# Kernel optimization log

Measured on AMD Instinct MI355X. Metric: run time of the kernel, lower is better.

Reference implementation:

```python
import jax, jax.numpy as jnp
import numpy as np

B, VOCAB, HIST, PEN_RANGE = 256, 128000, 512, 64


def setup_inputs() -> dict:
    key = jax.random.key(0)
    k1, k2, k3 = jax.random.split(key, 3)
    logits = jax.random.normal(k1, (B, VOCAB), dtype=jnp.float32)
    save_id = jax.random.randint(k2, (B, HIST), 0, VOCAB, dtype=jnp.int64)
    penalty_value = jax.random.uniform(k3, (1,), dtype=jnp.float32)
    return {
        "logits": logits,
        "save_id": save_id,
        "penalty_value": penalty_value,
        "penalty_range": PEN_RANGE,
    }


def reference(logits, save_id, penalty_value, penalty_range):
    # target_indices = save_id[:, -penalty_range:]  -> [B, R]
    idx = save_id[:, -penalty_range:]
    # gather logits at idx, multiply by penalty, scatter back (out-of-place)
    penalized = jnp.take_along_axis(logits, idx, axis=1) * penalty_value  # [B, R]
    rows = jnp.arange(logits.shape[0])[:, None]  # [B, 1]
    return logits.at[rows, idx].set(penalized)
```

## Files before the change

### kernel.cpp

```cpp
#include <hip/hip_runtime.h>

#define VOCAB 128000
#define HIST 512
#define ROW_F4 (VOCAB / 4)
#define CHUNKS_PER_ROW 8
#define CHUNK_F4 (ROW_F4 / CHUNKS_PER_ROW)
#define CHUNK_FLOATS (CHUNK_F4 * 4)

typedef float f32x4 __attribute__((ext_vector_type(4)));

__global__ __launch_bounds__(256)
void APPLY_PENALTY_5909874999394_fused(const f32x4* __restrict__ logits4,
                                       const float* __restrict__ logits,
                                       const int* __restrict__ save_id,
                                       const float* __restrict__ pval,
                                       const int* __restrict__ prange,
                                       f32x4* __restrict__ out4,
                                       float* __restrict__ out) {
    const int bid   = blockIdx.x;
    const int row   = bid >> 3;
    const int chunk = bid & 7;
    const long rowoff4 = (long)row * ROW_F4;
    const int  c0_4 = chunk * CHUNK_F4;

    for (int j = threadIdx.x; j < CHUNK_F4; j += 256) {
        f32x4 v = __builtin_nontemporal_load(&logits4[rowoff4 + c0_4 + j]);
        out4[rowoff4 + c0_4 + j] = v;
    }

    __syncthreads();

    const int pr = *prange;
    const float p = *pval;
    const int lo = c0_4 * 4;
    const int hi = lo + CHUNK_FLOATS;
    const int base = row * HIST + (HIST - pr);
    const long rowoff = (long)row * VOCAB;
    for (int k = threadIdx.x; k < pr; k += 256) {
        const int idx = save_id[base + k];
        if (idx >= lo && idx < hi)
            out[rowoff + idx] = logits[rowoff + idx] * p;
    }
}

extern "C" void kernel_launch(void* const* d_in, const int* in_sizes, int n_in,
                              void* d_out, int out_size, void* d_ws, size_t ws_size,
                              hipStream_t stream) {
    const float* logits  = (const float*)d_in[0];
    const int*   save_id = (const int*)d_in[1];
    const float* pval    = (const float*)d_in[2];
    const int*   prange  = (const int*)d_in[3];
    float* out = (float*)d_out;

    const int rows = out_size / VOCAB;
    const int grid = rows * CHUNKS_PER_ROW;
    APPLY_PENALTY_5909874999394_fused<<<grid, 256, 0, stream>>>(
        (const f32x4*)logits, logits, save_id, pval, prange,
        (f32x4*)out, out);
}
```

Baseline: 49.19 us.

## Apply penalty in-register via shared bitmap during single-pass copy

Each block first loads its share of the penalty indices and builds a shared-memory bitmap of which positions in its 5120-float chunk are penalized. It then streams the chunk once, multiplying the flagged lanes before storing. This removes the second scattered read-modify-write pass and the post-copy barrier, so each element is written only once. The grid also grows from 8 to 25 chunks per row with a fixed 5 float4 loads per thread. The index loading assumes penalty_range is at most 512, and the nontemporal load hint is dropped.

```diff
diff --git a/kernel.cpp b/kernel.cpp
--- a/kernel.cpp
+++ b/kernel.cpp
@@ -3,43 +3,62 @@
 #define VOCAB 128000
 #define HIST 512
 #define ROW_F4 (VOCAB / 4)
-#define CHUNKS_PER_ROW 8
-#define CHUNK_F4 (ROW_F4 / CHUNKS_PER_ROW)
+#define CHUNKS_PER_ROW 25
+#define CHUNK_F4 1280
 #define CHUNK_FLOATS (CHUNK_F4 * 4)
+#define CHUNK_WORDS (CHUNK_FLOATS / 32)
+#define F4_PER_THREAD 5
 
 typedef float f32x4 __attribute__((ext_vector_type(4)));
 
 __global__ __launch_bounds__(256)
 void APPLY_PENALTY_5909874999394_fused(const f32x4* __restrict__ logits4,
-                                       const float* __restrict__ logits,
                                        const int* __restrict__ save_id,
                                        const float* __restrict__ pval,
                                        const int* __restrict__ prange,
-                                       f32x4* __restrict__ out4,
-                                       float* __restrict__ out) {
+                                       f32x4* __restrict__ out4) {
     const int bid   = blockIdx.x;
-    const int row   = bid >> 3;
-    const int chunk = bid & 7;
-    const long rowoff4 = (long)row * ROW_F4;
-    const int  c0_4 = chunk * CHUNK_F4;
-
-    for (int j = threadIdx.x; j < CHUNK_F4; j += 256) {
-        f32x4 v = __builtin_nontemporal_load(&logits4[rowoff4 + c0_4 + j]);
-        out4[rowoff4 + c0_4 + j] = v;
-    }
-
-    __syncthreads();
+    const int row   = bid / CHUNKS_PER_ROW;
+    const int chunk = bid % CHUNKS_PER_ROW;
+    const int tid   = threadIdx.x;
 
     const int pr = *prange;
     const float p = *pval;
-    const int lo = c0_4 * 4;
-    const int hi = lo + CHUNK_FLOATS;
+    const int lo = chunk * CHUNK_FLOATS;
+
+    __shared__ unsigned bm[CHUNK_WORDS];
+
+    int id0 = -1, id1 = -1;
     const int base = row * HIST + (HIST - pr);
-    const long rowoff = (long)row * VOCAB;
-    for (int k = threadIdx.x; k < pr; k += 256) {
-        const int idx = save_id[base + k];
-        if (idx >= lo && idx < hi)
-            out[rowoff + idx] = logits[rowoff + idx] * p;
+    if (tid < pr)       id0 = save_id[base + tid];
+    if (tid + 256 < pr) id1 = save_id[base + tid + 256];
+
+    if (tid < CHUNK_WORDS) bm[tid] = 0;
+    __syncthreads();
+
+    if (id0 >= lo && id0 < lo + CHUNK_FLOATS) {
+        const int b = id0 - lo;
+        atomicOr(&bm[b >> 5], 1u << (b & 31));
+    }
+    if (id1 >= lo && id1 < lo + CHUNK_FLOATS) {
+        const int b = id1 - lo;
+        atomicOr(&bm[b >> 5], 1u << (b & 31));
+    }
+    __syncthreads();
+
+    const long base4 = (long)row * ROW_F4 + (long)chunk * CHUNK_F4;
+    #pragma unroll
+    for (int i = 0; i < F4_PER_THREAD; ++i) {
+        const int f = tid + i * 256;
+        f32x4 v = logits4[base4 + f];
+        const unsigned nib = (bm[f >> 3] >> ((f & 7) * 4)) & 0xFu;
+        if (nib) {
+            if (nib & 1u) v.x *= p;
+            if (nib & 2u) v.y *= p;
+            if (nib & 4u) v.z *= p;
+            if (nib & 8u) v.w *= p;
+        }
+        out4[base4 + f] = v;
     }
 }
 
@@ -55,6 +74,5 @@
     const int rows = out_size / VOCAB;
     const int grid = rows * CHUNKS_PER_ROW;
     APPLY_PENALTY_5909874999394_fused<<<grid, 256, 0, stream>>>(
-        (const f32x4*)logits, logits, save_id, pval, prange,
-        (f32x4*)out, out);
+        (const f32x4*)logits, save_id, pval, prange, (f32x4*)out);
 }
```

Measured after the change: 44.94 us. 1.09x faster.
